# Kernel optimization log

Measured on AMD Instinct MI355X. Metric: run time of the kernel, lower is better.

## Reference

```python
import jax, jax.numpy as jnp
import numpy as np

N_NODES = 50000
N_EDGES = 800000
FEAT = 256
HID = 64
OUT = 40


def setup_inputs() -> dict:
    key = jax.random.key(0)
    ks = jax.random.split(key, 5)
    x = jax.random.normal(ks[0], (N_NODES, FEAT), dtype=jnp.float32)
    edge_index = jax.random.randint(ks[1], (2, N_EDGES), 0, N_NODES, dtype=jnp.int64)
    # Glorot-style init for GCN linear weights
    W1 = jax.random.normal(ks[2], (FEAT, HID), dtype=jnp.float32) * (1.0 / np.sqrt(FEAT))
    b1 = jnp.zeros((HID,), dtype=jnp.float32)
    W2 = jax.random.normal(ks[3], (HID, OUT), dtype=jnp.float32) * (1.0 / np.sqrt(HID))
    b2 = jnp.zeros((OUT,), dtype=jnp.float32)
    return {"x": x, "edge_index": edge_index, "W1": W1, "b1": b1, "W2": W2, "b2": b2}


def _gcn_conv(h, W, b, src, dst, norm, n_nodes):
    # GCNConv: linear transform first (reduces message width), then
    # symmetric-normalized gather-scale-scatter aggregation.
    h = h @ W  # [N, out]
    msg = h[src] * norm[:, None]  # [E+N, out] gather + scale
    agg = jax.ops.segment_sum(msg, dst, num_segments=n_nodes)  # scatter-add
    return agg + b


def reference(x, edge_index, W1, b1, W2, b2):
    n = x.shape[0]
    # add self loops (GCNConv default add_self_loops=True)
    loops = jnp.arange(n, dtype=edge_index.dtype)
    src = jnp.concatenate([edge_index[0], loops])
    dst = jnp.concatenate([edge_index[1], loops])
    # symmetric normalization: deg computed on A + I (in-degree at dst)
    deg = jax.ops.segment_sum(jnp.ones_like(dst, dtype=x.dtype), dst, num_segments=n)
    dinv = jax.lax.rsqrt(deg)  # deg >= 1 due to self loops
    norm = dinv[src] * dinv[dst]  # [E+N]

    h = jax.nn.relu(_gcn_conv(x, W1, b1, src, dst, norm, n))
    # dropout is identity in eval mode (reference baseline)
    h = _gcn_conv(h, W2, b2, src, dst, norm, n)
    return jax.nn.log_softmax(h, axis=1)
```

## Files before the change

### kernel.cpp

```cpp
#include <hip/hip_runtime.h>
#include <hip/hip_bf16.h>


constexpr int NN   = 50000;
constexpr int NNP  = 50048;
constexpr int ZR   = 50000;
constexpr int NE   = 800000;
constexpr int FEAT = 256;
constexpr int HID  = 64;
constexpr int OUTD = 40;
constexpr int NC   = (NN + 255) / 256;
constexpr int NBUK = NC;
constexpr int MAXB = 4608;
constexpr int RPT  = MAXB / 256;
constexpr int FCH  = 2048;
constexpr int NCH  = (NE + FCH - 1) / FCH;
constexpr int GB   = NNP / 64;

typedef short bf16x8 __attribute__((ext_vector_type(8)));
typedef float f32x4  __attribute__((ext_vector_type(4)));
typedef float f32x2  __attribute__((ext_vector_type(2)));

__device__ __forceinline__ float b2f(__hip_bfloat16 v) { return __bfloat162float(v); }
__device__ __forceinline__ float bflo(unsigned u) { return __uint_as_float(u << 16); }
__device__ __forceinline__ float bfhi(unsigned u) { return __uint_as_float(u & 0xffff0000u); }
__device__ __forceinline__ unsigned short f2bu(float f) {
    __hip_bfloat16 h = __float2bfloat16(f);
    return *(unsigned short*)&h;
}
__device__ __forceinline__ unsigned pack2bf(float a, float b) {
    return (unsigned)f2bu(a) | ((unsigned)f2bu(b) << 16);
}
__device__ __forceinline__ float loadF(const void* p, int i, bool f32) {
    return f32 ? ((const float*)p)[i] : b2f(((const __hip_bfloat16*)p)[i]);
}
__device__ __forceinline__ int loadE(const int* ei, int e, int row, bool i64) {
    long long idx = (long long)row * NE + e;
    return i64 ? ei[2 * idx] : ei[idx];
}
__device__ __forceinline__ bf16x8 pack8(float4 a, float4 b) {
    bf16x8 r;
    r[0] = (short)f2bu(a.x); r[1] = (short)f2bu(a.y);
    r[2] = (short)f2bu(a.z); r[3] = (short)f2bu(a.w);
    r[4] = (short)f2bu(b.x); r[5] = (short)f2bu(b.y);
    r[6] = (short)f2bu(b.z); r[7] = (short)f2bu(b.w);
    return r;
}

#if __has_builtin(__builtin_amdgcn_cvt_pk_f32_fp8) && __has_builtin(__builtin_amdgcn_cvt_pk_fp8_f32)
__device__ __forceinline__ void unpack_fp8x4(unsigned u, float& f0, float& f1,
                                             float& f2, float& f3) {
    f32x2 lo = __builtin_amdgcn_cvt_pk_f32_fp8((int)u, false);
    f32x2 hi = __builtin_amdgcn_cvt_pk_f32_fp8((int)u, true);
    f0 = lo[0]; f1 = lo[1]; f2 = hi[0]; f3 = hi[1];
}
__device__ __forceinline__ unsigned pack_fp8x4(float a, float b, float c, float d) {
    int v = 0;
    v = __builtin_amdgcn_cvt_pk_fp8_f32(a, b, v, false);
    v = __builtin_amdgcn_cvt_pk_fp8_f32(c, d, v, true);
    return (unsigned)v;
}
#else
__device__ __forceinline__ float dec8(unsigned b) {
    return __uint_as_float(((b & 0x80u) << 24) | ((b & 0x7fu) << 20)) * 0x1p120f;
}
__device__ __forceinline__ void unpack_fp8x4(unsigned u, float& f0, float& f1,
                                             float& f2, float& f3) {
    f0 = dec8(u & 0xff); f1 = dec8((u >> 8) & 0xff);
    f2 = dec8((u >> 16) & 0xff); f3 = dec8(u >> 24);
}
__device__ __forceinline__ unsigned enc8(float f) {
    float a = fabsf(f) * 0x1p-120f;
    unsigned ub = __float_as_uint(a);
    unsigned lsb = (ub >> 20) & 1u;
    ub += 0x7FFFFu + lsb;
    unsigned v = (ub >> 20) & 0x7fu;
    if (v > 0x7e) v = 0x7e;
    return v | ((__float_as_uint(f) >> 24) & 0x80u);
}
__device__ __forceinline__ unsigned pack_fp8x4(float a, float b, float c, float d) {
    return enc8(a) | (enc8(b) << 8) | (enc8(c) << 16) | (enc8(d) << 24);
}
#endif

__global__ __launch_bounds__(256) void k_zero(const unsigned* __restrict__ xw,
                                              const int* __restrict__ ew,
                                              int* flags, int* bcur,
                                              unsigned* __restrict__ h2pad) {
    const int t = threadIdx.x;
    bcur[t] = 0;
    if (t < 16) h2pad[t] = 0;
    if (t < 64) {
        int outliers = 0;
#pragma unroll
        for (int k = t; k < 256; k += 64) {
            int e = (xw[k] >> 7) & 0xFF;
            if (e < 100 || e > 140) outliers++;
        }
        int nz = 0;
        if (t < 32) nz = (ew[1 + 2 * t] != 0) ? 1 : 0;
#pragma unroll
        for (int off = 32; off; off >>= 1) {
            outliers += __shfl_down(outliers, off, 64);
            nz       += __shfl_down(nz, off, 64);
        }
        if (t == 0) {
            flags[0] = (outliers > 64) ? 1 : 0;
            flags[1] = (nz == 0) ? 1 : 0;
        }
    }
}

__global__ __launch_bounds__(256) void k_bingemm(const int* __restrict__ ei,
                                                 const int* __restrict__ flags,
                                                 int* __restrict__ bcur,
                                                 unsigned* __restrict__ binned,
                                                 const void* __restrict__ xb,
                                                 const void* __restrict__ W1,
                                                 unsigned short* __restrict__ h1u) {
    __shared__ __align__(16) unsigned char smem[64 * 264 * 2];
    const bool f32 = flags[0] != 0;
    const int t = threadIdx.x;

    if (blockIdx.x < NCH) {
        const bool i64 = flags[1] != 0;
        int* histL = (int*)smem;
        int* lbase = histL + 256;
        unsigned* recL = (unsigned*)(lbase + 256);
        histL[t] = 0;
        __syncthreads();
        int dk[8], sk[8], lk[8];
        const int e0 = blockIdx.x * FCH;
#pragma unroll
        for (int k = 0; k < 8; k++) {
            int e = e0 + k * 256 + t;
            if (e < NE) {
                dk[k] = loadE(ei, e, 1, i64);
                sk[k] = loadE(ei, e, 0, i64);
                lk[k] = atomicAdd(&histL[dk[k] >> 8], 1);
            } else {
                dk[k] = -1;
            }
        }
        __syncthreads();
        const int v = histL[t];
        lbase[t] = v;
        __syncthreads();
        for (int off = 1; off < 256; off <<= 1) {
            int tmp = (t >= off) ? lbase[t - off] : 0;
            __syncthreads();
            lbase[t] += tmp;
            __syncthreads();
        }
        int excl = lbase[t] - v;
        __syncthreads();
        lbase[t] = excl;
        __syncthreads();
#pragma unroll
        for (int k = 0; k < 8; k++) {
            if (dk[k] >= 0) {
                int b = dk[k] >> 8;
                recL[lbase[b] + lk[k]] = (unsigned)(sk[k] | ((dk[k] & 0xff) << 16));
            }
        }
        int gbase = (v > 0) ? atomicAdd(&bcur[t], v) : 0;
        __syncthreads();
        const int lb = lbase[t];
        for (int i = 0; i < v; i++) {
            int off = gbase + i;
            if (off < MAXB) binned[t * MAXB + off] = recL[lb + i];
        }
        return;
    }

    const int bid = blockIdx.x - NCH;
    unsigned short* wt16 = (unsigned short*)smem;
    if (f32) {
        const float* wf = (const float*)W1;
        for (int i = t * 4; i < FEAT * HID; i += 1024) {
            float4 w = *(const float4*)(wf + i);
            int k = i >> 6, n0 = i & 63;
            wt16[(n0 + 0) * 264 + k] = f2bu(w.x);
            wt16[(n0 + 1) * 264 + k] = f2bu(w.y);
            wt16[(n0 + 2) * 264 + k] = f2bu(w.z);
            wt16[(n0 + 3) * 264 + k] = f2bu(w.w);
        }
    } else {
        const unsigned short* wu = (const unsigned short*)W1;
        for (int i = t * 4; i < FEAT * HID; i += 1024) {
            ushort4 w = *(const ushort4*)(wu + i);
            int k = i >> 6, n0 = i & 63;
            wt16[(n0 + 0) * 264 + k] = w.x;
            wt16[(n0 + 1) * 264 + k] = w.y;
            wt16[(n0 + 2) * 264 + k] = w.z;
            wt16[(n0 + 3) * 264 + k] = w.w;
        }
    }
    const int wv = t >> 6, lane = t & 63, l15 = lane & 15, quad = lane >> 4;
    const int gr = bid * 64 + wv * 16 + l15;
    const bool rowok = gr < NN;
    f32x4 acc[4];
#pragma unroll
    for (int nt = 0; nt < 4; nt++) acc[nt] = (f32x4){0.f, 0.f, 0.f, 0.f};
    __syncthreads();

    if (f32) {
        const float* xr = (const float*)xb + (size_t)gr * FEAT + quad * 8;
        float4 z4 = make_float4(0, 0, 0, 0);
        float4 c0 = rowok ? *(const float4*)xr : z4;
        float4 c1 = rowok ? *(const float4*)(xr + 4) : z4;
#pragma unroll
        for (int ks = 0; ks < 8; ks++) {
            float4 n0 = z4, n1 = z4;
            if (ks < 7 && rowok) {
                n0 = *(const float4*)(xr + (ks + 1) * 32);
                n1 = *(const float4*)(xr + (ks + 1) * 32 + 4);
            }
            bf16x8 a = pack8(c0, c1);
            const unsigned short* wk = wt16 + ks * 32 + quad * 8;
#pragma unroll
            for (int nt = 0; nt < 4; nt++) {
                bf16x8 b = *(const bf16x8*)(wk + (size_t)(nt * 16 + l15) * 264);
                acc[nt] = __builtin_amdgcn_mfma_f32_16x16x32_bf16(a, b, acc[nt], 0, 0, 0);
            }
            c0 = n0; c1 = n1;
        }
    } else {
        const unsigned short* xr = (const unsigned short*)xb + (size_t)gr * FEAT + quad * 8;
        bf16x8 zz = (bf16x8){0, 0, 0, 0, 0, 0, 0, 0};
        bf16x8 cur = rowok ? *(const bf16x8*)xr : zz;
#pragma unroll
        for (int ks = 0; ks < 8; ks++) {
            bf16x8 nxt = zz;
            if (ks < 7 && rowok) nxt = *(const bf16x8*)(xr + (ks + 1) * 32);
            const unsigned short* wk = wt16 + ks * 32 + quad * 8;
#pragma unroll
            for (int nt = 0; nt < 4; nt++) {
                bf16x8 b = *(const bf16x8*)(wk + (size_t)(nt * 16 + l15) * 264);
                acc[nt] = __builtin_amdgcn_mfma_f32_16x16x32_bf16(cur, b, acc[nt], 0, 0, 0);
            }
            cur = nxt;
        }
    }
    const int rbase = bid * 64 + wv * 16 + quad * 4;
#pragma unroll
    for (int r = 0; r < 4; r++) {
        int grow = rbase + r;
#pragma unroll
        for (int nt = 0; nt < 4; nt++)
            h1u[(size_t)grow * HID + nt * 16 + l15] = f2bu(acc[nt][r]);
    }
}

__global__ __launch_bounds__(256) void k_rankfill(const int* __restrict__ bcur,
                                                  const unsigned* __restrict__ binned,
                                                  int* __restrict__ pp,
                                                  int* __restrict__ cnt,
                                                  float* __restrict__ dinv,
                                                  int* __restrict__ row_start,
                                                  unsigned short* __restrict__ csr16) {
    __shared__ int h[256];
    __shared__ int s[256];
    __shared__ int ppL[256];
    __shared__ unsigned short csrL[MAXB];
    const int t = threadIdx.x, b = blockIdx.x;
    h[t] = 0;
    __syncthreads();
    const int cntb = min(bcur[b], MAXB);
    const int base = b * MAXB;
    unsigned recA[RPT];
    int rkA[RPT];
#pragma unroll
    for (int j = 0; j < RPT; j++) {
        int pos = j * 256 + t;
        if (pos < cntb) {
            unsigned rec = binned[base + pos];
            recA[j] = rec;
            rkA[j] = atomicAdd(&h[(rec >> 16) & 0xff], 1);
        }
    }
    __syncthreads();
    int pv = (t < NC) ? min(bcur[t], MAXB) : 0;
    ppL[t] = pv;
    __syncthreads();
    for (int off = 1; off < 256; off <<= 1) {
        int tmp = (t >= off) ? ppL[t - off] : 0;
        __syncthreads();
        ppL[t] += tmp;
        __syncthreads();
    }
    int pexcl = ppL[t] - pv;
    __syncthreads();
    ppL[t] = pexcl;
    __syncthreads();
    if (b == 0) pp[t] = pexcl;
    const int i = b * 256 + t;
    const int v = h[t];
    if (i < NN) {
        cnt[i] = v;
        dinv[i] = rsqrtf(1.0f + (float)v);
    }
    s[t] = v;
    __syncthreads();
    for (int off = 1; off < 256; off <<= 1) {
        int tmp = (t >= off) ? s[t - off] : 0;
        __syncthreads();
        s[t] += tmp;
        __syncthreads();
    }
    int excl = s[t] - v;
    if (i < NN) row_start[i] = excl;
    __syncthreads();
    s[t] = excl;
    __syncthreads();
#pragma unroll
    for (int j = 0; j < RPT; j++) {
        int pos = j * 256 + t;
        if (pos < cntb) {
            int lo = (recA[j] >> 16) & 0xff;
            csrL[s[lo] + rkA[j]] = (unsigned short)(recA[j] & 0xffff);
        }
    }
    __syncthreads();
    const int ppb = ppL[b];
    for (int pos = t; pos < cntb; pos += 256)
        csr16[ppb + pos] = csrL[pos];
}

__global__ __launch_bounds__(256) void k_scale(const float* __restrict__ dinv,
                                               unsigned* __restrict__ h1q) {
    const int stride = gridDim.x * 256;
    for (int i = blockIdx.x * 256 + threadIdx.x; i < NNP * 32; i += stride) {
        unsigned u = h1q[i];
        int row = i >> 5;
        float dv = (row < NN) ? dinv[row] : 0.f;
        h1q[i] = pack2bf(bflo(u) * dv, bfhi(u) * dv);
    }
}

__global__ __launch_bounds__(256, 4) void k_gather1f(const uint2* __restrict__ h1v,
                                                  const float* __restrict__ dinv,
                                                  const int* __restrict__ row_start,
                                                  const int* __restrict__ pp,
                                                  const int* __restrict__ cnt,
                                                  const unsigned short* __restrict__ csr16,
                                                  const void* __restrict__ W2,
                                                  const void* __restrict__ b1,
                                                  const int* __restrict__ flags,
                                                  unsigned* __restrict__ h2f) {
    __shared__ __align__(16) float w2t[OUTD * 68];
    __shared__ __align__(16) float gbuf[16 * 68];
    __shared__ __align__(16) float obuf[16][40];
    __shared__ float dns[16];
    const bool f32 = flags[0] != 0;
    const int t = threadIdx.x;
    for (int i = t; i < HID * OUTD; i += 256) {
        int c = i >> 6, k = i & 63;
        w2t[c * 68 + k] = loadF(W2, (size_t)k * OUTD + c, f32);
    }
    const int nl = t >> 4, l16 = t & 15;
    const int n = blockIdx.x * 16 + nl;
    const float dn = dinv[n];
    uint2 u0 = h1v[n * 16 + l16];
    float a0 = bflo(u0.x), a1 = bfhi(u0.x), a2 = bflo(u0.y), a3 = bfhi(u0.y);
    float e0 = 0.f, e1 = 0.f, e2 = 0.f, e3 = 0.f;
    const int rs = row_start[n] + pp[n >> 8], c = cnt[n];
    for (int base = 0; base < c; base += 16) {
        int rem = c - base;
        int sv = (l16 < rem) ? (int)csr16[rs + base + l16] : ZR;
        uint2 b[8], d[8];
#pragma unroll
        for (int j = 0; j < 8; j++) {
            int s = __shfl(sv, j, 16);
            b[j] = h1v[(s << 4) | l16];
        }
#pragma unroll
        for (int j = 0; j < 8; j++) {
            int s = __shfl(sv, j + 8, 16);
            d[j] = h1v[(s << 4) | l16];
        }
#pragma unroll
        for (int j = 0; j < 8; j++) {
            a0 += bflo(b[j].x); a1 += bfhi(b[j].x);
            a2 += bflo(b[j].y); a3 += bfhi(b[j].y);
            e0 += bflo(d[j].x); e1 += bfhi(d[j].x);
            e2 += bflo(d[j].y); e3 += bfhi(d[j].y);
        }
    }
    int cb = 4 * l16;
    float g0 = fmaxf(dn * (a0 + e0) + loadF(b1, cb, f32), 0.f);
    float g1 = fmaxf(dn * (a1 + e1) + loadF(b1, cb + 1, f32), 0.f);
    float g2 = fmaxf(dn * (a2 + e2) + loadF(b1, cb + 2, f32), 0.f);
    float g3 = fmaxf(dn * (a3 + e3) + loadF(b1, cb + 3, f32), 0.f);
    *(float4*)(gbuf + nl * 68 + cb) = make_float4(g0, g1, g2, g3);
    if (l16 == 0) dns[nl] = dn;
    __syncthreads();
    for (int idx = t; idx < 16 * OUTD; idx += 256) {
        int node = idx / OUTD, col = idx % OUTD;
        const float4* gp = (const float4*)(gbuf + node * 68);
        const float4* wp = (const float4*)(w2t + col * 68);
        float o = 0.f;
#pragma unroll 4
        for (int k4 = 0; k4 < 16; k4++) {
            float4 a = gp[k4], b = wp[k4];
            o += a.x * b.x + a.y * b.y + a.z * b.z + a.w * b.w;
        }
        obuf[node][col] = o * dns[node];
    }
    __syncthreads();
    if (t < 160) {
        int node = t / 10, dw = t % 10;
        const float* op = obuf[node] + dw * 4;
        h2f[(blockIdx.x * 16 + node) * 16 + dw] =
            pack_fp8x4(op[0], op[1], op[2], op[3]);
    }
}

__global__ __launch_bounds__(256, 4) void k_gather2(const unsigned* __restrict__ h2f,
                                                 const float* __restrict__ dinv,
                                                 const int* __restrict__ row_start,
                                                 const int* __restrict__ pp,
                                                 const int* __restrict__ cnt,
                                                 const unsigned short* __restrict__ csr16,
                                                 const void* __restrict__ b2,
                                                 const int* __restrict__ flags,
                                                 void* __restrict__ out) {
    const bool f32 = flags[0] != 0;
    const int t = threadIdx.x;
    const int nl = t >> 4, l16 = t & 15;
    const int n = blockIdx.x * 16 + nl;
    const bool act = l16 < 10;
    const float dn = dinv[n];
    const int lclamp = act ? l16 : 9;
    float a0, a1, a2, a3;
    unpack_fp8x4(h2f[n * 16 + lclamp], a0, a1, a2, a3);
    float e0 = 0.f, e1 = 0.f, e2 = 0.f, e3 = 0.f;
    const int rs = row_start[n] + pp[n >> 8], c = cnt[n];
    for (int base = 0; base < c; base += 16) {
        int rem = c - base;
        int sv = (l16 < rem) ? (int)csr16[rs + base + l16] : ZR;
        unsigned b[8], d[8];
#pragma unroll
        for (int j = 0; j < 8; j++) {
            int s = __shfl(sv, j, 16);
            b[j] = h2f[(s << 4) + lclamp];
        }
#pragma unroll
        for (int j = 0; j < 8; j++) {
            int s = __shfl(sv, j + 8, 16);
            d[j] = h2f[(s << 4) + lclamp];
        }
#pragma unroll
        for (int j = 0; j < 8; j++) {
            float x0, x1, x2, x3, y0, y1, y2, y3;
            unpack_fp8x4(b[j], x0, x1, x2, x3);
            unpack_fp8x4(d[j], y0, y1, y2, y3);
            a0 += x0; a1 += x1; a2 += x2; a3 += x3;
            e0 += y0; e1 += y1; e2 += y2; e3 += y3;
        }
    }
    int cb = 4 * l16;
    float v0 = -3.0e38f, v1 = -3.0e38f, v2 = -3.0e38f, v3 = -3.0e38f;
    if (act) {
        v0 = dn * (a0 + e0) + loadF(b2, cb, f32);
        v1 = dn * (a1 + e1) + loadF(b2, cb + 1, f32);
        v2 = dn * (a2 + e2) + loadF(b2, cb + 2, f32);
        v3 = dn * (a3 + e3) + loadF(b2, cb + 3, f32);
    }
    float mx = fmaxf(fmaxf(v0, v1), fmaxf(v2, v3));
#pragma unroll
    for (int off = 8; off; off >>= 1) mx = fmaxf(mx, __shfl_xor(mx, off, 16));
    float ev = act ? expf(v0 - mx) + expf(v1 - mx) + expf(v2 - mx) + expf(v3 - mx) : 0.f;
#pragma unroll
    for (int off = 8; off; off >>= 1) ev += __shfl_xor(ev, off, 16);
    float lg = logf(ev);
    if (act) {
        float r0 = v0 - mx - lg, r1 = v1 - mx - lg;
        float r2 = v2 - mx - lg, r3 = v3 - mx - lg;
        if (f32) {
            *(float4*)((float*)out + (size_t)n * OUTD + cb) = make_float4(r0, r1, r2, r3);
        } else {
            ((uint2*)out)[(size_t)n * 10 + l16] = make_uint2(pack2bf(r0, r1), pack2bf(r2, r3));
        }
    }
}

extern "C" void kernel_launch(void* const* d_in, const int* in_sizes, int n_in,
                              void* d_out, int out_size, void* d_ws, size_t ws_size,
                              hipStream_t stream) {
    const void* x  = d_in[0];
    const int*  ei = (const int*)d_in[1];
    const void* W1 = d_in[2];
    const void* b1 = d_in[3];
    const void* W2 = d_in[4];
    const void* b2 = d_in[5];

    float* ws        = (float*)d_ws;
    int*   flags     = (int*)ws;
    float* dinv      = ws + 16;
    int*   cnt       = (int*)(dinv + 50048);
    int*   row_start = cnt + 50048;
    int*   pp        = row_start + 50048;
    int*   bcur      = pp + 256;
    unsigned* binned = (unsigned*)(bcur + 256);
    unsigned short* csr16 = (unsigned short*)(binned + NBUK * MAXB);
    unsigned short* h1u   = csr16 + NE;
    unsigned* h2f = (unsigned*)(h1u + (size_t)NNP * HID);
    unsigned* h2pad = h2f + (size_t)ZR * 16;

    k_zero    <<<1, 256, 0, stream>>>((const unsigned*)x, ei, flags, bcur, h2pad);
    k_bingemm <<<NCH + GB, 256, 0, stream>>>(ei, flags, bcur, binned, x, W1, h1u);
    k_rankfill<<<NBUK, 256, 0, stream>>>(bcur, binned, pp, cnt, dinv, row_start, csr16);
    k_scale   <<<512, 256, 0, stream>>>(dinv, (unsigned*)h1u);
    k_gather1f<<<NN / 16, 256, 0, stream>>>((const uint2*)h1u, dinv, row_start, pp, cnt,
                                            csr16, W2, b1, flags, h2f);
    k_gather2 <<<NN / 16, 256, 0, stream>>>(h2f, dinv, row_start, pp, cnt, csr16,
                                            b2, flags, d_out);
}
```

Before: 192.6 us.

## Fold flag detection into bin kernel and fuse scaling into rankfill

Removes the single-block k_zero launch. Every block of k_bingemm now recomputes the dtype and index-width flags into shared memory, and bcur is cleared with a memset. The per-node dinv scaling of h1 moves from a separate k_scale kernel into the tail of the rankfill kernel, which uses the per-bucket degree histogram it already holds. The bin scatter is also reworked so all threads copy records cooperatively, with the bucket id packed into the record, instead of each thread serially writing one bucket's run. This removes two kernel launches and a full extra pass over h1, at the cost of redundant flag reads in every block and a dependency between the scaling and the rankfill work.

```diff
diff --git a/kernel.cpp b/kernel.cpp
--- a/kernel.cpp
+++ b/kernel.cpp
@@ -83,13 +83,18 @@
 }
 #endif
 
-__global__ __launch_bounds__(256) void k_zero(const unsigned* __restrict__ xw,
-                                              const int* __restrict__ ew,
-                                              int* flags, int* bcur,
-                                              unsigned* __restrict__ h2pad) {
+__global__ __launch_bounds__(256) void k_bingemm(const int* __restrict__ ei,
+                                                 const unsigned* __restrict__ xw,
+                                                 int* __restrict__ flags,
+                                                 int* __restrict__ bcur,
+                                                 unsigned* __restrict__ binned,
+                                                 const void* __restrict__ W1,
+                                                 unsigned short* __restrict__ h1u) {
+    __shared__ __align__(16) unsigned char smem[64 * 264 * 2];
+    __shared__ int flagsL[2];
     const int t = threadIdx.x;
-    bcur[t] = 0;
-    if (t < 16) h2pad[t] = 0;
+    const void* xb = (const void*)xw;
+
     if (t < 64) {
         int outliers = 0;
 #pragma unroll
@@ -98,35 +103,30 @@
             if (e < 100 || e > 140) outliers++;
         }
         int nz = 0;
-        if (t < 32) nz = (ew[1 + 2 * t] != 0) ? 1 : 0;
+        if (t < 32) nz = (ei[1 + 2 * t] != 0) ? 1 : 0;
 #pragma unroll
         for (int off = 32; off; off >>= 1) {
             outliers += __shfl_down(outliers, off, 64);
             nz       += __shfl_down(nz, off, 64);
         }
         if (t == 0) {
-            flags[0] = (outliers > 64) ? 1 : 0;
-            flags[1] = (nz == 0) ? 1 : 0;
-        }
-    }
-}
-
-__global__ __launch_bounds__(256) void k_bingemm(const int* __restrict__ ei,
-                                                 const int* __restrict__ flags,
-                                                 int* __restrict__ bcur,
-                                                 unsigned* __restrict__ binned,
-                                                 const void* __restrict__ xb,
-                                                 const void* __restrict__ W1,
-                                                 unsigned short* __restrict__ h1u) {
-    __shared__ __align__(16) unsigned char smem[64 * 264 * 2];
-    const bool f32 = flags[0] != 0;
-    const int t = threadIdx.x;
+            flagsL[0] = (outliers > 64) ? 1 : 0;
+            flagsL[1] = (nz == 0) ? 1 : 0;
+            if (blockIdx.x == 0) {
+                flags[0] = flagsL[0];
+                flags[1] = flagsL[1];
+            }
+        }
+    }
+    __syncthreads();
+    const bool f32 = flagsL[0] != 0;
+    const bool i64 = flagsL[1] != 0;
 
     if (blockIdx.x < NCH) {
-        const bool i64 = flags[1] != 0;
         int* histL = (int*)smem;
         int* lbase = histL + 256;
-        unsigned* recL = (unsigned*)(lbase + 256);
+        int* gbL   = lbase + 256;
+        unsigned* recL = (unsigned*)(gbL + 256);
         histL[t] = 0;
         __syncthreads();
         int dk[8], sk[8], lk[8];
@@ -160,15 +160,18 @@
         for (int k = 0; k < 8; k++) {
             if (dk[k] >= 0) {
                 int b = dk[k] >> 8;
-                recL[lbase[b] + lk[k]] = (unsigned)(sk[k] | ((dk[k] & 0xff) << 16));
+                recL[lbase[b] + lk[k]] =
+                    (unsigned)(sk[k] | ((dk[k] & 0xff) << 16) | (b << 24));
             }
         }
-        int gbase = (v > 0) ? atomicAdd(&bcur[t], v) : 0;
-        __syncthreads();
-        const int lb = lbase[t];
-        for (int i = 0; i < v; i++) {
-            int off = gbase + i;
-            if (off < MAXB) binned[t * MAXB + off] = recL[lb + i];
+        gbL[t] = (v > 0) ? atomicAdd(&bcur[t], v) : 0;
+        __syncthreads();
+        const int totalCnt = min(FCH, NE - e0);
+        for (int pos = t; pos < totalCnt; pos += 256) {
+            unsigned rec = recL[pos];
+            int b = rec >> 24;
+            int off = gbL[b] + (pos - lbase[b]);
+            if (off < MAXB) binned[b * MAXB + off] = rec & 0xffffff;
         }
         return;
     }
@@ -252,19 +255,22 @@
     }
 }
 
-__global__ __launch_bounds__(256) void k_rankfill(const int* __restrict__ bcur,
+__global__ __launch_bounds__(256) void k_rankfillscale(const int* __restrict__ bcur,
                                                   const unsigned* __restrict__ binned,
                                                   int* __restrict__ pp,
                                                   int* __restrict__ cnt,
                                                   float* __restrict__ dinv,
                                                   int* __restrict__ row_start,
-                                                  unsigned short* __restrict__ csr16) {
+                                                  unsigned short* __restrict__ csr16,
+                                                  unsigned* __restrict__ h1q,
+                                                  unsigned* __restrict__ h2f) {
     __shared__ int h[256];
     __shared__ int s[256];
     __shared__ int ppL[256];
     __shared__ unsigned short csrL[MAXB];
     const int t = threadIdx.x, b = blockIdx.x;
     h[t] = 0;
+    if (b == 0 && t < 16) h2f[ZR * 16 + t] = 0;
     __syncthreads();
     const int cntb = min(bcur[b], MAXB);
     const int base = b * MAXB;
@@ -325,16 +331,15 @@
     const int ppb = ppL[b];
     for (int pos = t; pos < cntb; pos += 256)
         csr16[ppb + pos] = csrL[pos];
-}
-
-__global__ __launch_bounds__(256) void k_scale(const float* __restrict__ dinv,
-                                               unsigned* __restrict__ h1q) {
-    const int stride = gridDim.x * 256;
-    for (int i = blockIdx.x * 256 + threadIdx.x; i < NNP * 32; i += stride) {
-        unsigned u = h1q[i];
-        int row = i >> 5;
-        float dv = (row < NN) ? dinv[row] : 0.f;
-        h1q[i] = pack2bf(bflo(u) * dv, bfhi(u) * dv);
+    const int row0 = b * 256;
+    for (int k = t; k < 256 * 32; k += 256) {
+        int rl = k >> 5;
+        int row = row0 + rl;
+        if (row < NNP) {
+            float dv = (row < NN) ? rsqrtf(1.0f + (float)h[rl]) : 0.f;
+            unsigned u = h1q[row * 32 + (k & 31)];
+            h1q[row * 32 + (k & 31)] = pack2bf(bflo(u) * dv, bfhi(u) * dv);
+        }
     }
 }
 
@@ -506,12 +511,12 @@
     unsigned short* csr16 = (unsigned short*)(binned + NBUK * MAXB);
     unsigned short* h1u   = csr16 + NE;
     unsigned* h2f = (unsigned*)(h1u + (size_t)NNP * HID);
-    unsigned* h2pad = h2f + (size_t)ZR * 16;
-
-    k_zero    <<<1, 256, 0, stream>>>((const unsigned*)x, ei, flags, bcur, h2pad);
-    k_bingemm <<<NCH + GB, 256, 0, stream>>>(ei, flags, bcur, binned, x, W1, h1u);
-    k_rankfill<<<NBUK, 256, 0, stream>>>(bcur, binned, pp, cnt, dinv, row_start, csr16);
-    k_scale   <<<512, 256, 0, stream>>>(dinv, (unsigned*)h1u);
+
+    hipMemsetAsync(bcur, 0, 256 * sizeof(int), stream);
+    k_bingemm <<<NCH + GB, 256, 0, stream>>>(ei, (const unsigned*)x, flags, bcur,
+                                             binned, W1, h1u);
+    k_rankfillscale<<<NBUK, 256, 0, stream>>>(bcur, binned, pp, cnt, dinv, row_start,
+                                              csr16, (unsigned*)h1u, h2f);
     k_gather1f<<<NN / 16, 256, 0, stream>>>((const uint2*)h1u, dinv, row_start, pp, cnt,
                                             csr16, W2, b1, flags, h2f);
     k_gather2 <<<NN / 16, 256, 0, stream>>>(h2f, dinv, row_start, pp, cnt, csr16,
```

Measured after the change: 190.5 us. Within noise of the previous version (-1.1%).
